# Kernel optimization log

Measured on AMD Instinct MI355X. Metric: run time of the kernel, lower is better.

Reference implementation:

```python
import jax, jax.numpy as jnp
import numpy as np

NUM_HEADS = 16
HEAD_DIM = 64
MAX_REL = 128
NEG_INF = -1e30


def setup_inputs() -> dict:
    key = jax.random.key(0)
    ks = jax.random.split(key, 5)
    B, L, D = 2, 2048, 1024
    x = jax.random.normal(ks[0], (B, L, D), dtype=jnp.float32)
    key_padding_mask = jnp.zeros((B, L), dtype=bool)  # True = padded
    Wqkv = jax.random.normal(ks[1], (D, 3 * D), dtype=jnp.float32) * (D ** -0.5)
    bqkv = jnp.zeros((3 * D,), dtype=jnp.float32)
    Wout = jax.random.normal(ks[2], (D, D), dtype=jnp.float32) * (D ** -0.5)
    bout = jnp.zeros((D,), dtype=jnp.float32)
    bias_table = jax.random.normal(ks[3], (2 * MAX_REL + 1, NUM_HEADS), dtype=jnp.float32) * 0.02
    return {"x": x, "key_padding_mask": key_padding_mask, "Wqkv": Wqkv,
            "bqkv": bqkv, "Wout": Wout, "bout": bout, "bias_table": bias_table}


def _rel_bias(bias_table, L):
    # relative position index: clamp(k - q, -MAX_REL, MAX_REL) + MAX_REL -> [L, L]
    rel = jnp.arange(L)[None, :] - jnp.arange(L)[:, None]
    idx = jnp.clip(rel, -MAX_REL, MAX_REL) + MAX_REL
    return bias_table[idx].transpose(2, 0, 1)  # [H, L, L]


def reference(x, key_padding_mask, Wqkv, bqkv, Wout, bout, bias_table):
    B, L, D = x.shape
    H, hd = NUM_HEADS, HEAD_DIM
    qkv = x @ Wqkv + bqkv                      # [B, L, 3D]
    q, k, v = jnp.split(qkv, 3, axis=-1)
    q = q.reshape(B, L, H, hd).transpose(0, 2, 1, 3)  # [B, H, L, hd]
    k = k.reshape(B, L, H, hd).transpose(0, 2, 1, 3)
    v = v.reshape(B, L, H, hd).transpose(0, 2, 1, 3)
    scores = jnp.einsum('bhqd,bhkd->bhqk', q, k) * (hd ** -0.5)
    scores = scores + _rel_bias(bias_table, L)[None]   # [B, H, L, L]
    scores = jnp.where(key_padding_mask[:, None, None, :], NEG_INF, scores)
    attn = jax.nn.softmax(scores, axis=-1)
    out = jnp.einsum('bhqk,bhkd->bhqd', attn, v)       # [B, H, L, hd]
    out = out.transpose(0, 2, 1, 3).reshape(B, L, D)
    return out @ Wout + bout
```

## Files before the change

kernel.cpp:

```cpp
#include <hip/hip_runtime.h>
#include <hip/hip_bf16.h>
#include <stdint.h>

#define LSEQ 2048
#define BATCH 2
#define DMODEL 1024
#define NH 16
#define HD 64

typedef __attribute__((ext_vector_type(8))) short bf16x8;
typedef __attribute__((ext_vector_type(4))) float f32x4;

__device__ __forceinline__ short f2bf(float f) {
  union { float f; uint32_t u; } v; v.f = f;
  uint32_t r = v.u + 0x8000u;
  return (short)(r >> 16);
}

__device__ __forceinline__ uint32_t pack_bf16(float lo, float hi) {
  union { float f; uint32_t u; } a, b; a.f = lo; b.f = hi;
  uint32_t al = (a.u + 0x8000u) >> 16;
  uint32_t bh = (b.u + 0x8000u) & 0xFFFF0000u;
  return al | bh;
}

__device__ __forceinline__ float exp2_fast(float x) {
#if __has_builtin(__builtin_amdgcn_exp2f)
  return __builtin_amdgcn_exp2f(x);
#else
  float r; asm("v_exp_f32 %0, %1" : "=v"(r) : "v"(x)); return r;
#endif
}

__device__ __forceinline__ void gll16(const void* g, void* l) {
  __builtin_amdgcn_global_load_lds(
      (const __attribute__((address_space(1))) void*)g,
      (__attribute__((address_space(3))) void*)l, 16, 0, 0);
}

__global__ void cvt_bf16(const float* __restrict__ in, short* __restrict__ out, int n) {
  int i = (blockIdx.x * blockDim.x + threadIdx.x) * 4;
  if (i < n) {
    float4 v = *(const float4*)(in + i);
    short4 o;
    o.x = f2bf(v.x); o.y = f2bf(v.y); o.z = f2bf(v.z); o.w = f2bf(v.w);
    *(short4*)(out + i) = o;
  }
}

__global__ void transpose_cvt(const float* __restrict__ in, short* __restrict__ out,
                              int K, int N) {
  __shared__ float tile[32][33];
  int kb = blockIdx.x * 32, nb = blockIdx.y * 32;
  int tx = threadIdx.x & 31, ty = threadIdx.x >> 5;
  #pragma unroll
  for (int i = ty; i < 32; i += 8)
    tile[i][tx] = in[(size_t)(kb + i) * N + nb + tx];
  __syncthreads();
  #pragma unroll
  for (int i = ty; i < 32; i += 8)
    out[(size_t)(nb + i) * K + kb + tx] = f2bf(tile[tx][i]);
}

template <int EPI>
__global__ __launch_bounds__(256, 3) void gemm_bt(
    const short* __restrict__ A, const short* __restrict__ Bt,
    const float* __restrict__ bias, float* __restrict__ outf,
    short* __restrict__ q_out, short* __restrict__ k_out, short* __restrict__ v_out) {
  constexpr int K = 1024, BK = 32, NKT = K / BK;
  __shared__ short Als[2][128 * BK];
  __shared__ short Bls[2][128 * BK];
  const int tid = threadIdx.x;
  const int lane = tid & 63;
  const int m0 = blockIdx.x * 128;
  const int n0 = blockIdx.y * 128;
  const int wid = tid >> 6;
  const int wm = (wid >> 1) * 64, wn = (wid & 1) * 64;

  f32x4 acc[4][4] = {};

  auto stage = [&](int kt, int bbuf) {
    const int k0 = kt * BK;
    #pragma unroll
    for (int inst = 0; inst < 2; ++inst) {
      int c = inst * 256 + tid;
      int row = c >> 2, cc = (c & 3) * 8;
      gll16(A + (size_t)(m0 + row) * K + k0 + cc, &Als[bbuf][c * 8]);
      gll16(Bt + (size_t)(n0 + row) * K + k0 + cc, &Bls[bbuf][c * 8]);
    }
  };

  stage(0, 0);

  for (int kt = 0; kt < NKT; ++kt) {
    const int bb = kt & 1;
    asm volatile("s_waitcnt vmcnt(0)" ::: "memory");
    __builtin_amdgcn_s_barrier();
    if (kt < NKT - 1) stage(kt + 1, bb ^ 1);

    bf16x8 af[4], bfv[4];
    #pragma unroll
    for (int m = 0; m < 4; ++m)
      af[m] = *(const bf16x8*)(&Als[bb][0] + (wm + m * 16 + (lane & 15)) * BK + (lane >> 4) * 8);
    #pragma unroll
    for (int n = 0; n < 4; ++n)
      bfv[n] = *(const bf16x8*)(&Bls[bb][0] + (wn + n * 16 + (lane & 15)) * BK + (lane >> 4) * 8);
    #pragma unroll
    for (int m = 0; m < 4; ++m)
      #pragma unroll
      for (int n = 0; n < 4; ++n)
        acc[m][n] = __builtin_amdgcn_mfma_f32_16x16x32_bf16(af[m], bfv[n], acc[m][n], 0, 0, 0);
  }

  #pragma unroll
  for (int m = 0; m < 4; ++m) {
    #pragma unroll
    for (int n = 0; n < 4; ++n) {
      #pragma unroll
      for (int r = 0; r < 4; ++r) {
        int row = m0 + wm + m * 16 + (lane >> 4) * 4 + r;
        int col = n0 + wn + n * 16 + (lane & 15);
        float val = acc[m][n][r] + bias[col];
        if (EPI == 1) {
          outf[(size_t)row * DMODEL + col] = val;
        } else {
          int b = row >> 11, l = row & 2047;
          int which = col >> 10, rem = col & 1023;
          int hn = rem >> 6, d = rem & 63;
          size_t bh = (size_t)b * NH + hn;
          if (which == 0)       q_out[(bh * LSEQ + l) * HD + d] = f2bf(val * 0.1803368801f);
          else if (which == 1)  k_out[(bh * LSEQ + l) * HD + d] = f2bf(val);
          else                  v_out[(bh * HD + d) * LSEQ + l] = f2bf(val);
        }
      }
    }
  }
}

__global__ __launch_bounds__(256, 2) void attn_kernel(
    const short* __restrict__ qb, const short* __restrict__ kb,
    const short* __restrict__ vtb, const unsigned char* __restrict__ kpm,
    const float* __restrict__ bias_table, short* __restrict__ ob) {
  constexpr int NT = LSEQ / 64;
  __shared__ short Kls[2][64 * 64];
  __shared__ short Vls[2][64 * 64];
  __shared__ short Pls[4][32 * 64];
  __shared__ float biasc[257];
  __shared__ unsigned mbits_s;

  const int tid = threadIdx.x, lane = tid & 63, wid = tid >> 6;
  const int g = lane >> 4, c = lane & 15;
  const int lin = blockIdx.x;
  const int swz = (lin & 7) * 64 + (lin >> 3);
  const int q0 = (swz & 15) * 128;
  const int h = (swz >> 4) & 15;
  const int b = swz >> 8;
  const size_t bh = (size_t)b * NH + h;
  const short* qbase = qb + bh * LSEQ * HD;
  const short* kbase = kb + bh * LSEQ * HD;
  const short* vbase = vtb + bh * HD * LSEQ;
  const unsigned char* kpmb = kpm + (size_t)b * LSEQ;

  bf16x8 qf[2][2];
  #pragma unroll
  for (int qg = 0; qg < 2; ++qg)
    #pragma unroll
    for (int ks = 0; ks < 2; ++ks) {
      int qrow = q0 + wid * 32 + qg * 16 + c;
      qf[qg][ks] = *(const bf16x8*)(qbase + (size_t)qrow * HD + ks * 32 + g * 8);
    }

  if (tid < 32) {
    const uint4* mp = (const uint4*)(kpmb + tid * 64);
    uint4 m0 = mp[0], m1 = mp[1], m2 = mp[2], m3 = mp[3];
    unsigned anyb = m0.x | m0.y | m0.z | m0.w | m1.x | m1.y | m1.z | m1.w |
                    m2.x | m2.y | m2.z | m2.w | m3.x | m3.y | m3.z | m3.w;
    unsigned long long bal = __ballot(anyb != 0);
    if (tid == 0) mbits_s = (unsigned)bal;
  }
  for (int i = tid; i < 257; i += 256) biasc[i] = bias_table[i * NH + h] * 1.44269504f;
  __syncthreads();
  const unsigned mbits = mbits_s;
  const float cb_lo = biasc[0], cb_hi = biasc[256];

  auto stage = [&](int t, int bbuf) {
    const int kv0s = t * 64;
    #pragma unroll
    for (int inst = 0; inst < 2; ++inst) {
      int cc0 = inst * 256 + tid;
      int row = cc0 >> 3, cc = cc0 & 7;
      int scc = cc ^ (row & 7);
      gll16(kbase + (size_t)(kv0s + row) * HD + scc * 8, &Kls[bbuf][cc0 * 8]);
      gll16(vbase + (size_t)row * LSEQ + kv0s + scc * 8, &Vls[bbuf][cc0 * 8]);
    }
  };

  f32x4 o[4][2], l_acc[2];
  #pragma unroll
  for (int nt = 0; nt < 4; ++nt)
    #pragma unroll
    for (int qg = 0; qg < 2; ++qg) o[nt][qg] = (f32x4){0.f, 0.f, 0.f, 0.f};
  l_acc[0] = (f32x4){0.f, 0.f, 0.f, 0.f};
  l_acc[1] = (f32x4){0.f, 0.f, 0.f, 0.f};

  bf16x8 onesf;
  #pragma unroll
  for (int j = 0; j < 8; ++j) onesf[j] = (short)0x3F80;

  char* pw = (char*)&Pls[wid][0];
  const int c7s = (c & 7) << 4;

  stage(0, 0);

  for (int t = 0; t < NT; ++t) {
    const int bb = t & 1;
    const int kv0 = t * 64;
    asm volatile("s_waitcnt vmcnt(0)" ::: "memory");
    __builtin_amdgcn_s_barrier();
    if (t < NT - 1) stage(t + 1, bb ^ 1);

    f32x4 st[4][2];
    #pragma unroll
    for (int nt = 0; nt < 4; ++nt) {
      f32x4 a0 = {}, a1 = {};
      #pragma unroll
      for (int ks = 0; ks < 2; ++ks) {
        int krow = nt * 16 + c;
        int kbyte = ks * 64 + g * 16;
        const bf16x8 kf =
            *(const bf16x8*)((const char*)&Kls[bb][0] + krow * 128 + (kbyte ^ c7s));
        a0 = __builtin_amdgcn_mfma_f32_16x16x32_bf16(kf, qf[0][ks], a0, 0, 0, 0);
        a1 = __builtin_amdgcn_mfma_f32_16x16x32_bf16(kf, qf[1][ks], a1, 0, 0, 0);
      }
      st[nt][0] = a0; st[nt][1] = a1;
    }

    const int dw = kv0 - q0 - wid * 32;
    if (dw >= 160 || dw <= -192) {
      const float cb = dw > 0 ? cb_hi : cb_lo;
      #pragma unroll
      for (int nt = 0; nt < 4; ++nt)
        #pragma unroll
        for (int qg = 0; qg < 2; ++qg)
          #pragma unroll
          for (int r = 0; r < 4; ++r) st[nt][qg][r] += cb;
    } else {
      #pragma unroll
      for (int nt = 0; nt < 4; ++nt)
        #pragma unroll
        for (int qg = 0; qg < 2; ++qg) {
          const int base = dw + nt * 16 + g * 4 - qg * 16 - c;
          #pragma unroll
          for (int r = 0; r < 4; ++r) {
            int rel = base + r;
            rel = rel < -128 ? -128 : (rel > 128 ? 128 : rel);
            st[nt][qg][r] += biasc[rel + 128];
          }
        }
    }
    if (mbits & (1u << t)) {
      #pragma unroll
      for (int nt = 0; nt < 4; ++nt)
        #pragma unroll
        for (int r = 0; r < 4; ++r) {
          float mk = kpmb[kv0 + nt * 16 + g * 4 + r] ? -1e30f : 0.f;
          st[nt][0][r] += mk;
          st[nt][1][r] += mk;
        }
    }

    #pragma unroll
    for (int qg = 0; qg < 2; ++qg)
      #pragma unroll
      for (int nt = 0; nt < 4; ++nt) {
        uint32_t p01 = pack_bf16(exp2_fast(st[nt][qg][0]), exp2_fast(st[nt][qg][1]));
        uint32_t p23 = pack_bf16(exp2_fast(st[nt][qg][2]), exp2_fast(st[nt][qg][3]));
        uint2 w; w.x = p01; w.y = p23;
        *(uint2*)(pw + (qg * 16 + c) * 128 + ((nt * 32 + g * 8) ^ c7s)) = w;
      }

    asm volatile("s_waitcnt lgkmcnt(0)" ::: "memory");
    __builtin_amdgcn_sched_barrier(0);

    #pragma unroll
    for (int ks = 0; ks < 2; ++ks) {
      const int pbyte = ks * 64 + g * 16;
      bf16x8 pa0 = *(const bf16x8*)(pw + c * 128 + (pbyte ^ c7s));
      bf16x8 pa1 = *(const bf16x8*)(pw + (16 + c) * 128 + (pbyte ^ c7s));
      l_acc[0] = __builtin_amdgcn_mfma_f32_16x16x32_bf16(pa0, onesf, l_acc[0], 0, 0, 0);
      l_acc[1] = __builtin_amdgcn_mfma_f32_16x16x32_bf16(pa1, onesf, l_acc[1], 0, 0, 0);
      #pragma unroll
      for (int nt = 0; nt < 4; ++nt) {
        int vrow = nt * 16 + c;
        const bf16x8 vf =
            *(const bf16x8*)((const char*)&Vls[bb][0] + vrow * 128 + (pbyte ^ c7s));
        o[nt][0] = __builtin_amdgcn_mfma_f32_16x16x32_bf16(pa0, vf, o[nt][0], 0, 0, 0);
        o[nt][1] = __builtin_amdgcn_mfma_f32_16x16x32_bf16(pa1, vf, o[nt][1], 0, 0, 0);
      }
    }
  }

  #pragma unroll
  for (int qg = 0; qg < 2; ++qg)
    #pragma unroll
    for (int r = 0; r < 4; ++r) {
      float inv = 1.f / l_acc[qg][r];
      int qrow = q0 + wid * 32 + qg * 16 + g * 4 + r;
      size_t obase = ((size_t)b * LSEQ + qrow) * DMODEL + (size_t)h * HD;
      #pragma unroll
      for (int nt = 0; nt < 4; ++nt)
        ob[obase + nt * 16 + c] = f2bf(o[nt][qg][r] * inv);
    }
}

extern "C" void kernel_launch(void* const* d_in, const int* in_sizes, int n_in,
                              void* d_out, int out_size, void* d_ws, size_t ws_size,
                              hipStream_t stream) {
  (void)in_sizes; (void)n_in; (void)out_size; (void)ws_size;
  const float* x = (const float*)d_in[0];
  const unsigned char* kpm = (const unsigned char*)d_in[1];
  const float* Wqkv = (const float*)d_in[2];
  const float* bqkv = (const float*)d_in[3];
  const float* Wout = (const float*)d_in[4];
  const float* bout = (const float*)d_in[5];
  const float* btab = (const float*)d_in[6];
  float* out = (float*)d_out;

  short* ws = (short*)d_ws;
  short* xbf   = ws;
  short* wqkvT = xbf + 4194304;
  short* woutT = wqkvT + 3145728;
  short* qbuf  = woutT + 1048576;
  short* kbuf  = qbuf + 4194304;
  short* vtbuf = kbuf + 4194304;
  short* obuf  = vtbuf + 4194304;

  cvt_bf16<<<dim3(4096), dim3(256), 0, stream>>>(x, xbf, 4194304);
  transpose_cvt<<<dim3(32, 96), dim3(256), 0, stream>>>(Wqkv, wqkvT, 1024, 3072);
  transpose_cvt<<<dim3(32, 32), dim3(256), 0, stream>>>(Wout, woutT, 1024, 1024);

  gemm_bt<0><<<dim3(32, 24), dim3(256), 0, stream>>>(xbf, wqkvT, bqkv, nullptr,
                                                     qbuf, kbuf, vtbuf);
  attn_kernel<<<dim3(512), dim3(256), 0, stream>>>(qbuf, kbuf, vtbuf, kpm, btab, obuf);
  gemm_bt<1><<<dim3(32, 8), dim3(256), 0, stream>>>(obuf, woutT, bout, out,
                                                    nullptr, nullptr, nullptr);
}
```

Before: 134.3 us.

## Write V row-major from QKV GEMM, transpose separately; raise MFMA wave priority

The QKV GEMM epilogue now writes V in the same [bh, L, d] layout as Q and K, so its stores are coalesced along d instead of strided scatters along L. A new transpose16 kernel, staged through shared memory, turns that V into the transposed layout that attention expects, using obuf as scratch. s_setprio is also raised around the MFMA blocks in both the GEMM and attention kernels to favour matrix work when waves compete. The cost is one extra kernel launch plus an extra read and write of V.

```diff
diff --git a/kernel.cpp b/kernel.cpp
--- a/kernel.cpp
+++ b/kernel.cpp
@@ -60,6 +60,23 @@
   #pragma unroll
   for (int i = ty; i < 32; i += 8)
     out[(size_t)(nb + i) * K + kb + tx] = f2bf(tile[tx][i]);
+}
+
+__global__ void transpose16(const short* __restrict__ in, short* __restrict__ out) {
+  __shared__ short tile[32][33];
+  const int bhid = blockIdx.z;
+  const int lb = blockIdx.x * 32;
+  const int db = blockIdx.y * 32;
+  const short* ip = in + (size_t)bhid * LSEQ * HD;
+  short* op = out + (size_t)bhid * HD * LSEQ;
+  int tx = threadIdx.x & 31, ty = threadIdx.x >> 5;
+  #pragma unroll
+  for (int i = ty; i < 32; i += 8)
+    tile[i][tx] = ip[(size_t)(lb + i) * HD + db + tx];
+  __syncthreads();
+  #pragma unroll
+  for (int i = ty; i < 32; i += 8)
+    op[(size_t)(db + i) * LSEQ + lb + tx] = tile[tx][i];
 }
 
 template <int EPI>
@@ -105,11 +122,13 @@
     #pragma unroll
     for (int n = 0; n < 4; ++n)
       bfv[n] = *(const bf16x8*)(&Bls[bb][0] + (wn + n * 16 + (lane & 15)) * BK + (lane >> 4) * 8);
+    __builtin_amdgcn_s_setprio(1);
     #pragma unroll
     for (int m = 0; m < 4; ++m)
       #pragma unroll
       for (int n = 0; n < 4; ++n)
         acc[m][n] = __builtin_amdgcn_mfma_f32_16x16x32_bf16(af[m], bfv[n], acc[m][n], 0, 0, 0);
+    __builtin_amdgcn_s_setprio(0);
   }
 
   #pragma unroll
@@ -127,10 +146,10 @@
           int b = row >> 11, l = row & 2047;
           int which = col >> 10, rem = col & 1023;
           int hn = rem >> 6, d = rem & 63;
-          size_t bh = (size_t)b * NH + hn;
-          if (which == 0)       q_out[(bh * LSEQ + l) * HD + d] = f2bf(val * 0.1803368801f);
-          else if (which == 1)  k_out[(bh * LSEQ + l) * HD + d] = f2bf(val);
-          else                  v_out[(bh * HD + d) * LSEQ + l] = f2bf(val);
+          size_t idx = (((size_t)b * NH + hn) * LSEQ + l) * HD + d;
+          if (which == 0)       q_out[idx] = f2bf(val * 0.1803368801f);
+          else if (which == 1)  k_out[idx] = f2bf(val);
+          else                  v_out[idx] = f2bf(val);
         }
       }
     }
@@ -220,6 +239,7 @@
     if (t < NT - 1) stage(t + 1, bb ^ 1);
 
     f32x4 st[4][2];
+    __builtin_amdgcn_s_setprio(1);
     #pragma unroll
     for (int nt = 0; nt < 4; ++nt) {
       f32x4 a0 = {}, a1 = {};
@@ -234,6 +254,7 @@
       }
       st[nt][0] = a0; st[nt][1] = a1;
     }
+    __builtin_amdgcn_s_setprio(0);
 
     const int dw = kv0 - q0 - wid * 32;
     if (dw >= 160 || dw <= -192) {
@@ -282,6 +303,7 @@
     asm volatile("s_waitcnt lgkmcnt(0)" ::: "memory");
     __builtin_amdgcn_sched_barrier(0);
 
+    __builtin_amdgcn_s_setprio(1);
     #pragma unroll
     for (int ks = 0; ks < 2; ++ks) {
       const int pbyte = ks * 64 + g * 16;
@@ -298,6 +320,7 @@
         o[nt][1] = __builtin_amdgcn_mfma_f32_16x16x32_bf16(pa1, vf, o[nt][1], 0, 0, 0);
       }
     }
+    __builtin_amdgcn_s_setprio(0);
   }
 
   #pragma unroll
@@ -340,7 +363,8 @@
   transpose_cvt<<<dim3(32, 32), dim3(256), 0, stream>>>(Wout, woutT, 1024, 1024);
 
   gemm_bt<0><<<dim3(32, 24), dim3(256), 0, stream>>>(xbf, wqkvT, bqkv, nullptr,
-                                                     qbuf, kbuf, vtbuf);
+                                                     qbuf, kbuf, obuf);
+  transpose16<<<dim3(64, 2, 32), dim3(256), 0, stream>>>(obuf, vtbuf);
   attn_kernel<<<dim3(512), dim3(256), 0, stream>>>(qbuf, kbuf, vtbuf, kpm, btab, obuf);
   gemm_bt<1><<<dim3(32, 8), dim3(256), 0, stream>>>(obuf, woutT, bout, out,
                                                     nullptr, nullptr, nullptr);
```

Result: slower. 137.2 us (+2.2%).

## Double GEMM K-tile with XOR-swizzled LDS and raise MFMA wave priority

Applied to the files above, without the earlier changes.

The GEMM K tile grows from 32 to 64, which halves the number of barrier/stage iterations. LDS rows are XOR-swizzled by row so the 128-byte rows can be read without bank conflicts, and launch bounds drop from 3 to 2 blocks per CU to fit the doubled shared memory. s_setprio is also wrapped around the MFMA sections in both the GEMM and the attention kernel, so waves issuing matrix ops get scheduling priority. Costs: fewer resident blocks per CU and more LDS per block.

```diff
diff --git a/kernel.cpp b/kernel.cpp
--- a/kernel.cpp
+++ b/kernel.cpp
@@ -63,15 +63,16 @@
 }
 
 template <int EPI>
-__global__ __launch_bounds__(256, 3) void gemm_bt(
+__global__ __launch_bounds__(256, 2) void gemm_bt(
     const short* __restrict__ A, const short* __restrict__ Bt,
     const float* __restrict__ bias, float* __restrict__ outf,
     short* __restrict__ q_out, short* __restrict__ k_out, short* __restrict__ v_out) {
-  constexpr int K = 1024, BK = 32, NKT = K / BK;
+  constexpr int K = 1024, BK = 64, NKT = K / BK;
   __shared__ short Als[2][128 * BK];
   __shared__ short Bls[2][128 * BK];
   const int tid = threadIdx.x;
   const int lane = tid & 63;
+  const int c = lane & 15, g = lane >> 4;
   const int m0 = blockIdx.x * 128;
   const int n0 = blockIdx.y * 128;
   const int wid = tid >> 6;
@@ -82,11 +83,12 @@
   auto stage = [&](int kt, int bbuf) {
     const int k0 = kt * BK;
     #pragma unroll
-    for (int inst = 0; inst < 2; ++inst) {
-      int c = inst * 256 + tid;
-      int row = c >> 2, cc = (c & 3) * 8;
-      gll16(A + (size_t)(m0 + row) * K + k0 + cc, &Als[bbuf][c * 8]);
-      gll16(Bt + (size_t)(n0 + row) * K + k0 + cc, &Bls[bbuf][c * 8]);
+    for (int inst = 0; inst < 4; ++inst) {
+      int i = inst * 256 + tid;
+      int row = i >> 3, cg = i & 7;
+      int scc = cg ^ (row & 7);
+      gll16(A + (size_t)(m0 + row) * K + k0 + scc * 8, &Als[bbuf][i * 8]);
+      gll16(Bt + (size_t)(n0 + row) * K + k0 + scc * 8, &Bls[bbuf][i * 8]);
     }
   };
 
@@ -98,18 +100,28 @@
     __builtin_amdgcn_s_barrier();
     if (kt < NKT - 1) stage(kt + 1, bb ^ 1);
 
-    bf16x8 af[4], bfv[4];
-    #pragma unroll
-    for (int m = 0; m < 4; ++m)
-      af[m] = *(const bf16x8*)(&Als[bb][0] + (wm + m * 16 + (lane & 15)) * BK + (lane >> 4) * 8);
-    #pragma unroll
-    for (int n = 0; n < 4; ++n)
-      bfv[n] = *(const bf16x8*)(&Bls[bb][0] + (wn + n * 16 + (lane & 15)) * BK + (lane >> 4) * 8);
-    #pragma unroll
-    for (int m = 0; m < 4; ++m)
-      #pragma unroll
-      for (int n = 0; n < 4; ++n)
-        acc[m][n] = __builtin_amdgcn_mfma_f32_16x16x32_bf16(af[m], bfv[n], acc[m][n], 0, 0, 0);
+    #pragma unroll
+    for (int ks = 0; ks < 2; ++ks) {
+      const int kb = ks * 64 + g * 16;
+      bf16x8 af[4], bfv[4];
+      #pragma unroll
+      for (int m = 0; m < 4; ++m) {
+        int row = wm + m * 16 + c;
+        af[m] = *(const bf16x8*)((const char*)&Als[bb][0] + row * 128 + (kb ^ ((row & 7) << 4)));
+      }
+      #pragma unroll
+      for (int n = 0; n < 4; ++n) {
+        int row = wn + n * 16 + c;
+        bfv[n] = *(const bf16x8*)((const char*)&Bls[bb][0] + row * 128 + (kb ^ ((row & 7) << 4)));
+      }
+      __builtin_amdgcn_s_setprio(1);
+      #pragma unroll
+      for (int m = 0; m < 4; ++m)
+        #pragma unroll
+        for (int n = 0; n < 4; ++n)
+          acc[m][n] = __builtin_amdgcn_mfma_f32_16x16x32_bf16(af[m], bfv[n], acc[m][n], 0, 0, 0);
+      __builtin_amdgcn_s_setprio(0);
+    }
   }
 
   #pragma unroll
@@ -118,8 +130,8 @@
     for (int n = 0; n < 4; ++n) {
       #pragma unroll
       for (int r = 0; r < 4; ++r) {
-        int row = m0 + wm + m * 16 + (lane >> 4) * 4 + r;
-        int col = n0 + wn + n * 16 + (lane & 15);
+        int row = m0 + wm + m * 16 + g * 4 + r;
+        int col = n0 + wn + n * 16 + c;
         float val = acc[m][n][r] + bias[col];
         if (EPI == 1) {
           outf[(size_t)row * DMODEL + col] = val;
@@ -220,6 +232,7 @@
     if (t < NT - 1) stage(t + 1, bb ^ 1);
 
     f32x4 st[4][2];
+    __builtin_amdgcn_s_setprio(1);
     #pragma unroll
     for (int nt = 0; nt < 4; ++nt) {
       f32x4 a0 = {}, a1 = {};
@@ -234,6 +247,7 @@
       }
       st[nt][0] = a0; st[nt][1] = a1;
     }
+    __builtin_amdgcn_s_setprio(0);
 
     const int dw = kv0 - q0 - wid * 32;
     if (dw >= 160 || dw <= -192) {
@@ -282,6 +296,7 @@
     asm volatile("s_waitcnt lgkmcnt(0)" ::: "memory");
     __builtin_amdgcn_sched_barrier(0);
 
+    __builtin_amdgcn_s_setprio(1);
     #pragma unroll
     for (int ks = 0; ks < 2; ++ks) {
       const int pbyte = ks * 64 + g * 16;
@@ -298,6 +313,7 @@
         o[nt][1] = __builtin_amdgcn_mfma_f32_16x16x32_bf16(pa1, vf, o[nt][1], 0, 0, 0);
       }
     }
+    __builtin_amdgcn_s_setprio(0);
   }
 
   #pragma unroll
```

After: 136.4 us. No clear change (+1.6%).
